# Performance work log

Hardware: AMD Instinct MI355X
Metric: run time of the kernel (lower is better)

## Reference

```python
import jax, jax.numpy as jnp
import numpy as np

D = 768           # PTM hidden size
BS = 64           # block size
HEADS = D // BS   # 12 = bilinear blocks = EGAT heads = PTM attention heads
R = 97            # relation_num
B = 4; L = 1024; M = 48; NE = 24
P = NE * (NE - 1)
NEG = 0.2         # DGL EGATConv leaky_relu slope


def _make_hts():
    hh, tt = np.meshgrid(np.arange(NE), np.arange(NE), indexing='ij')
    keep = hh.reshape(-1) != tt.reshape(-1)
    return jnp.asarray(np.stack([hh.reshape(-1)[keep], tt.reshape(-1)[keep]], 0), jnp.int32)


def setup_inputs():
    key = jax.random.key(0)
    ks = jax.random.split(key, 20)
    context = jax.random.normal(ks[0], (B, L, D), jnp.float32) * 0.5
    att = jax.random.uniform(ks[1], (B, HEADS, L, L), jnp.float32)
    attention = att / att.sum(-1, keepdims=True)  # softmax-like rows
    mention_map = jnp.sort(jax.random.randint(ks[2], (B, M), 0, L, jnp.int32), axis=-1)
    assign = jnp.arange(M) % NE  # every entity owns >= 1 mention (avoids log(0))
    entity_map = jnp.tile(jax.nn.one_hot(assign, NE, dtype=jnp.float32).T[None], (B, 1, 1))
    hts = _make_hts()
    def lin(k, fi, fo):
        return jax.random.normal(k, (fi, fo), jnp.float32) * 0.02
    return dict(
        context=context, attention=attention, mention_map=mention_map,
        entity_map=entity_map, hts=hts,
        Whb=lin(ks[3], 2 * D, D), bhb=jnp.zeros((D,), jnp.float32),
        Wtb=lin(ks[4], 2 * D, D), btb=jnp.zeros((D,), jnp.float32),
        Wbin=lin(ks[5], D * BS, 2), bbin=jnp.zeros((2,), jnp.float32),
        Wrel=lin(ks[6], D * BS, R), brel=jnp.zeros((R,), jnp.float32),
        Wh=lin(ks[7], 2 * D, D), bh=jnp.zeros((D,), jnp.float32),
        Wt=lin(ks[8], 2 * D, D), bt=jnp.zeros((D,), jnp.float32),
        Wnode=lin(ks[9], D, HEADS * BS), Wni=lin(ks[10], D, HEADS * BS),
        Wfij=lin(ks[11], D, HEADS * BS), Wnj=lin(ks[12], D, HEADS * BS),
        attn_p=jax.random.normal(ks[13], (HEADS, BS), jnp.float32) * 0.1,
        egat_b=jnp.zeros((HEADS * BS,), jnp.float32),
    )


def _gbl(x1, x2, W, b):
    # group_biLinear: blockwise outer product then linear
    n = x1.shape[0]
    a = x1.reshape(n, HEADS, BS)
    c = x2.reshape(n, HEADS, BS)
    return jnp.einsum('nhi,nhj->nhij', a, c).reshape(n, -1) @ W + b


def reference(context, attention, mention_map, entity_map, hts,
              Whb, bhb, Wtb, btb, Wbin, bbin, Wrel, brel,
              Wh, bh, Wt, bt, Wnode, Wni, Wfij, Wnj, attn_p, egat_b):
    Bn = context.shape[0]
    bidx = jnp.arange(Bn)[:, None]
    # ---- get_ht: logsumexp mention->entity pooling ----
    men = context[bidx, mention_map]                                        # [B,M,D]
    entity = jnp.log(jnp.einsum('bnm,bmd->bnd', entity_map, jnp.exp(men)))  # [B,NE,D]
    h = entity[:, hts[0]].reshape(Bn * P, D)
    t = entity[:, hts[1]].reshape(Bn * P, D)
    # ---- context_pooling ----
    att_m = jnp.take_along_axis(attention, mention_map[:, None, :, None], axis=2)  # [B,H,M,L]
    cur = jnp.einsum('bnm,bhml->bhnl', entity_map, att_m)                   # [B,H,NE,L]
    cur = cur / (entity_map.sum(-1)[:, None, :, None] + 1e-20)
    ca = (cur[:, :, hts[0]] * cur[:, :, hts[1]]).sum(1)                     # [B,P,L]
    ca = ca / (ca.sum(-1, keepdims=True) + 1e-20)
    ci = jnp.einsum('bpl,bld->bpd', ca, context)                            # [B,P,D]
    ci_f = ci.reshape(Bn * P, D)
    # ---- binary classifier ----
    bin_h = jnp.tanh(jnp.concatenate([h, ci_f], -1) @ Whb + bhb)
    bin_t = jnp.tanh(jnp.concatenate([t, ci_f], -1) @ Wtb + btb)
    bin_res = _gbl(bin_h, bin_t, Wbin, bbin)                                # [B*P,2]
    # ---- graph build (masked uniform graph instead of ragged dgl graphs) ----
    mask = (jnp.argmax(bin_res, -1) == 1).reshape(Bn, P)                    # detached in torch
    src = jnp.concatenate([hts[0], jnp.arange(NE, dtype=hts.dtype)])        # self loops appended
    dst = jnp.concatenate([hts[1], jnp.arange(NE, dtype=hts.dtype)])

    def egat(nodes, ef, m):
        ef_all = jnp.concatenate([ef, jnp.zeros((NE, D), ef.dtype)], 0)     # zero self-loop feats
        m_all = jnp.concatenate([m, jnp.ones((NE,), bool)], 0)
        f_out = (nodes @ Wni)[src] + (nodes @ Wnj)[dst] + ef_all @ Wfij + egat_b
        f_out = f_out.reshape(-1, HEADS, BS)                                # [E,H,bs]
        score = (jax.nn.leaky_relu(f_out, NEG) * attn_p).sum(-1)            # [E,H]
        score = jnp.where(m_all[:, None], score, -1e30)
        smax = jax.ops.segment_max(score, dst, num_segments=NE)
        ex = jnp.exp(score - smax[dst]) * m_all[:, None]
        den = jax.ops.segment_sum(ex, dst, num_segments=NE)
        a = ex / (den[dst] + 1e-20)                                         # edge softmax per dst
        hsrc = (nodes @ Wnode).reshape(NE, HEADS, BS)
        nout = jax.ops.segment_sum(hsrc[src] * a[:, :, None], dst, num_segments=NE)
        return nout.reshape(NE, HEADS * BS), f_out[:P].reshape(P, HEADS * BS)

    node_out, ef_new = jax.vmap(egat)(entity, ci, mask)
    # ---- get_res: real edges take EGAT edge feats, non-edges keep context_info ----
    new_ci = jnp.where(mask[..., None], ef_new, ci).reshape(Bn * P, D)
    nh = node_out[:, hts[0]].reshape(Bn * P, D)
    nt = node_out[:, hts[1]].reshape(Bn * P, D)
    nh = jnp.tanh(jnp.concatenate([nh, new_ci], -1) @ Wh + bh)
    nt = jnp.tanh(jnp.concatenate([nt, new_ci], -1) @ Wt + bt)
    relation_res = _gbl(nh, nt, Wrel, brel)                                 # [B*P,97]
    return (bin_res, relation_res)
```

## Files before the change

kernel.cpp:

```cpp
#include <hip/hip_runtime.h>
#include <hip/hip_bf16.h>

#define Bn   4
#define Lq   1024
#define Dm   768
#define Mm   48
#define NEe  24
#define Pp   552
#define Ee   576
#define Hh   12
#define BSz  64
#define Rr   97
#define Nn   2208
#define NPAD 112
#define NEG_SLOPE 0.2f

typedef short bf16x8 __attribute__((ext_vector_type(8)));
typedef float f32x4  __attribute__((ext_vector_type(4)));

static __device__ __forceinline__ ushort f2b(float x) {
    __hip_bfloat16 h = __float2bfloat16(x);
    return *reinterpret_cast<ushort*>(&h);
}
static __device__ __forceinline__ float b2f(ushort h) {
    uint u = ((uint)h) << 16;
    return __uint_as_float(u);
}
static __device__ __forceinline__ void split2(float x, ushort& h, ushort& l) {
    h = f2b(x);
    l = f2b(x - b2f(h));
}

__global__ void k_entity(const float* __restrict__ ctx, const int* __restrict__ mmap,
                         const float* __restrict__ emap, float* __restrict__ entity,
                         ushort* __restrict__ entH, ushort* __restrict__ entL)
{
    int x = blockIdx.x;
    int b = x / NEe;
    int rows[8]; float wts[8]; int nnz = 0;
    for (int m = 0; m < Mm; ++m) {
        float w = emap[(long)x * Mm + m];
        if (w != 0.f && nnz < 8) { rows[nnz] = mmap[b * Mm + m]; wts[nnz] = w; ++nnz; }
    }
    const float* cbase = ctx + (long)b * Lq * Dm;
    for (int d = threadIdx.x; d < Dm; d += 256) {
        float s = 0.f;
        for (int z = 0; z < nnz; ++z) s += wts[z] * expf(cbase[(long)rows[z] * Dm + d]);
        float v = logf(s);
        entity[(long)x * Dm + d] = v;
        ushort hh, ll; split2(v, hh, ll);
        entH[(long)x * Dm + d] = hh;
        entL[(long)x * Dm + d] = ll;
    }
}

__global__ void k_cur(const float* __restrict__ att, const int* __restrict__ mmap,
                      const float* __restrict__ emap, float* __restrict__ cur)
{
    int x = blockIdx.x;
    int b = x / (Hh * NEe); int rem = x % (Hh * NEe);
    int h = rem / NEe;      int n = rem % NEe;
    float cnt = 0.f;
    int rows[8]; float wts[8]; int nnz = 0;
    for (int m = 0; m < Mm; ++m) {
        float w = emap[((long)b * NEe + n) * Mm + m];
        cnt += w;
        if (w != 0.f && nnz < 8) { rows[nnz] = mmap[b * Mm + m]; wts[nnz] = w; ++nnz; }
    }
    float inv = 1.f / (cnt + 1e-20f);
    const float* abase = att + ((long)b * Hh + h) * (long)Lq * Lq;
    float* obase = cur + (long)x * Lq;
    for (int l = threadIdx.x; l < Lq; l += 256) {
        float s = 0.f;
        for (int z = 0; z < nnz; ++z) s += wts[z] * abase[(long)rows[z] * Lq + l];
        obase[l] = s * inv;
    }
}

__global__ void k_ca(const float* __restrict__ cur, const int* __restrict__ hts,
                     ushort* __restrict__ caH, ushort* __restrict__ caL)
{
    int bp = blockIdx.x; int b = bp / Pp, p = bp % Pp;
    int n0 = hts[p], n1 = hts[Pp + p];
    __shared__ float red[256];
    float vals[4]; float lsum = 0.f;
    for (int t = 0; t < 4; ++t) {
        int l = threadIdx.x + t * 256;
        float v = 0.f;
        #pragma unroll
        for (int h = 0; h < Hh; ++h) {
            v += cur[(((long)b * Hh + h) * NEe + n0) * Lq + l] *
                 cur[(((long)b * Hh + h) * NEe + n1) * Lq + l];
        }
        vals[t] = v; lsum += v;
    }
    red[threadIdx.x] = lsum; __syncthreads();
    for (int s = 128; s > 0; s >>= 1) {
        if (threadIdx.x < s) red[threadIdx.x] += red[threadIdx.x + s];
        __syncthreads();
    }
    float inv = 1.f / (red[0] + 1e-20f);
    for (int t = 0; t < 4; ++t) {
        int l = threadIdx.x + t * 256;
        float v = vals[t] * inv;
        long idx = (long)bp * Lq + l;
        ushort hh, ll; split2(v, hh, ll);
        caH[idx] = hh; caL[idx] = ll;
    }
}

__global__ __launch_bounds__(256)
void k_gemm_split(const float* __restrict__ A, const float* __restrict__ W,
                  const float* __restrict__ bias, float* __restrict__ C,
                  int M, int N, int K, int lda, int ldw, int ldc,
                  long sA, long sW, long sC, int act)
{
    A += (long)blockIdx.z * sA;
    W += (long)blockIdx.z * sW;
    C += (long)blockIdx.z * sC;
    __shared__ ushort Ah[64][40], Al[64][40], Bh[64][40], Bl[64][40];
    const int tid = threadIdx.x;
    const int r0 = blockIdx.y * 64, c0 = blockIdx.x * 64;
    const int w = tid >> 6, l = tid & 63, lr = l & 15, lk = l >> 4;
    const int wr = (w >> 1) * 32, wc = (w & 1) * 32;
    f32x4 acc[2][2];
    #pragma unroll
    for (int m = 0; m < 2; ++m)
        #pragma unroll
        for (int n = 0; n < 2; ++n) acc[m][n] = (f32x4){0.f, 0.f, 0.f, 0.f};

    const int ar  = tid >> 3;
    const int kq  = (tid & 7) * 4;
    const int bkk = tid >> 4;
    const int cc4 = (tid & 15) * 4;
    const float4 z4 = make_float4(0.f, 0.f, 0.f, 0.f);

    for (int k0 = 0; k0 < K; k0 += 32) {
        #pragma unroll
        for (int s = 0; s < 2; ++s) {
            int r = ar + s * 32;
            int gr = r0 + r;
            float4 v = (gr < M) ? *(const float4*)&A[(long)gr * lda + k0 + kq] : z4;
            ushort h0, l0, h1, l1;
            split2(v.x, h0, l0); split2(v.y, h1, l1);
            *(uint*)&Ah[r][kq]     = (uint)h0 | ((uint)h1 << 16);
            *(uint*)&Al[r][kq]     = (uint)l0 | ((uint)l1 << 16);
            split2(v.z, h0, l0); split2(v.w, h1, l1);
            *(uint*)&Ah[r][kq + 2] = (uint)h0 | ((uint)h1 << 16);
            *(uint*)&Al[r][kq + 2] = (uint)l0 | ((uint)l1 << 16);
        }
        #pragma unroll
        for (int s = 0; s < 2; ++s) {
            int kk = bkk + s * 16;
            float4 v = *(const float4*)&W[(long)(k0 + kk) * ldw + c0 + cc4];
            ushort hh, ll;
            split2(v.x, hh, ll); Bh[cc4 + 0][kk] = hh; Bl[cc4 + 0][kk] = ll;
            split2(v.y, hh, ll); Bh[cc4 + 1][kk] = hh; Bl[cc4 + 1][kk] = ll;
            split2(v.z, hh, ll); Bh[cc4 + 2][kk] = hh; Bl[cc4 + 2][kk] = ll;
            split2(v.w, hh, ll); Bh[cc4 + 3][kk] = hh; Bl[cc4 + 3][kk] = ll;
        }
        __syncthreads();
        bf16x8 fah[2], fal[2], fbh[2], fbl[2];
        #pragma unroll
        for (int m = 0; m < 2; ++m) {
            fah[m] = *(const bf16x8*)&Ah[wr + m * 16 + lr][lk * 8];
            fal[m] = *(const bf16x8*)&Al[wr + m * 16 + lr][lk * 8];
        }
        #pragma unroll
        for (int n = 0; n < 2; ++n) {
            fbh[n] = *(const bf16x8*)&Bh[wc + n * 16 + lr][lk * 8];
            fbl[n] = *(const bf16x8*)&Bl[wc + n * 16 + lr][lk * 8];
        }
        #pragma unroll
        for (int m = 0; m < 2; ++m)
            #pragma unroll
            for (int n = 0; n < 2; ++n) {
                acc[m][n] = __builtin_amdgcn_mfma_f32_16x16x32_bf16(fal[m], fbh[n], acc[m][n], 0, 0, 0);
                acc[m][n] = __builtin_amdgcn_mfma_f32_16x16x32_bf16(fah[m], fbl[n], acc[m][n], 0, 0, 0);
                acc[m][n] = __builtin_amdgcn_mfma_f32_16x16x32_bf16(fah[m], fbh[n], acc[m][n], 0, 0, 0);
            }
        __syncthreads();
    }
    #pragma unroll
    for (int m = 0; m < 2; ++m) {
        #pragma unroll
        for (int q = 0; q < 4; ++q) {
            int gr = r0 + wr + m * 16 + lk * 4 + q;
            if (gr >= M) continue;
            #pragma unroll
            for (int n = 0; n < 2; ++n) {
                int gc = c0 + wc + n * 16 + lr;
                float v = acc[m][n][q] + (bias ? bias[gc] : 0.f);
                if (act) v = tanhf(v);
                C[(long)gr * ldc + gc] = v;
            }
        }
    }
}

__global__ __launch_bounds__(256)
void k_gemm3_64(const ushort* __restrict__ AH, const ushort* __restrict__ AL,
                const ushort* __restrict__ BH, const ushort* __restrict__ BL,
                const float* __restrict__ bias, float* __restrict__ C,
                ushort* __restrict__ Ch, ushort* __restrict__ Cl,
                int M, int N, int K, int ldc, int act,
                long sA, long sB, long sC)
{
    AH += blockIdx.z * sA; AL += blockIdx.z * sA;
    BH += blockIdx.z * sB; BL += blockIdx.z * sB;
    C  += blockIdx.z * sC;
    ushort* ChB = Ch ? Ch + blockIdx.z * sC : (ushort*)nullptr;
    ushort* ClB = Cl ? Cl + blockIdx.z * sC : (ushort*)nullptr;
    __shared__ ushort AsH[64][40], AsL[64][40], BsH[64][40], BsL[64][40];
    const int tid = threadIdx.x;
    const int r0 = blockIdx.y * 64, c0 = blockIdx.x * 64;
    const int w = tid >> 6, l = tid & 63, lr = l & 15, lk = l >> 4;
    const int wr = (w >> 1) * 32, wc = (w & 1) * 32;
    f32x4 acc[2][2];
    #pragma unroll
    for (int m = 0; m < 2; ++m)
        #pragma unroll
        for (int n = 0; n < 2; ++n) acc[m][n] = (f32x4){0.f, 0.f, 0.f, 0.f};

    const int srow = tid >> 2, scb = (tid & 1) * 16;
    const bool doB = (tid >> 1) & 1;
    const bool ok = doB ? (c0 + srow < N) : (r0 + srow < M);
    const long g = doB ? (long)(c0 + srow) : (long)(r0 + srow);
    const ushort* pH = (doB ? BH : AH) + (ok ? g : 0) * (long)K;
    const ushort* pL = (doB ? BL : AL) + (ok ? g : 0) * (long)K;
    ushort (*dH)[40] = doB ? BsH : AsH;
    ushort (*dL)[40] = doB ? BsL : AsL;
    const uint4 z4 = make_uint4(0, 0, 0, 0);
    for (int k0 = 0; k0 < K; k0 += 32) {
        int kc = k0 + scb;
        *(uint4*)&dH[srow][scb]     = ok ? *(const uint4*)&pH[kc]     : z4;
        *(uint4*)&dH[srow][scb + 8] = ok ? *(const uint4*)&pH[kc + 8] : z4;
        *(uint4*)&dL[srow][scb]     = ok ? *(const uint4*)&pL[kc]     : z4;
        *(uint4*)&dL[srow][scb + 8] = ok ? *(const uint4*)&pL[kc + 8] : z4;
        __syncthreads();
        bf16x8 ah[2], al_[2], bh[2], bl_[2];
        #pragma unroll
        for (int m = 0; m < 2; ++m) {
            ah[m]  = *(const bf16x8*)&AsH[wr + m * 16 + lr][lk * 8];
            al_[m] = *(const bf16x8*)&AsL[wr + m * 16 + lr][lk * 8];
        }
        #pragma unroll
        for (int n = 0; n < 2; ++n) {
            bh[n]  = *(const bf16x8*)&BsH[wc + n * 16 + lr][lk * 8];
            bl_[n] = *(const bf16x8*)&BsL[wc + n * 16 + lr][lk * 8];
        }
        #pragma unroll
        for (int m = 0; m < 2; ++m)
            #pragma unroll
            for (int n = 0; n < 2; ++n) {
                acc[m][n] = __builtin_amdgcn_mfma_f32_16x16x32_bf16(al_[m], bh[n], acc[m][n], 0, 0, 0);
                acc[m][n] = __builtin_amdgcn_mfma_f32_16x16x32_bf16(ah[m], bl_[n], acc[m][n], 0, 0, 0);
                acc[m][n] = __builtin_amdgcn_mfma_f32_16x16x32_bf16(ah[m], bh[n], acc[m][n], 0, 0, 0);
            }
        __syncthreads();
    }
    #pragma unroll
    for (int m = 0; m < 2; ++m) {
        #pragma unroll
        for (int q = 0; q < 4; ++q) {
            int gr = r0 + wr + m * 16 + lk * 4 + q;
            if (gr >= M) continue;
            #pragma unroll
            for (int n = 0; n < 2; ++n) {
                int gc = c0 + wc + n * 16 + lr;
                float v = acc[m][n][q] + (bias ? bias[gc] : 0.f);
                if (act) v = tanhf(v);
                long oi = (long)gr * ldc + gc;
                C[oi] = v;
                if (ChB) { ushort hh, ll; split2(v, hh, ll); ChB[oi] = hh; ClB[oi] = ll; }
            }
        }
    }
}

__global__ __launch_bounds__(256)
void k_gemm3_cat64(const ushort* __restrict__ ndH, const ushort* __restrict__ ndL,
                   const ushort* __restrict__ ftH, const ushort* __restrict__ ftL,
                   const int* __restrict__ hts,
                   const ushort* __restrict__ BH0, const ushort* __restrict__ BL0,
                   const ushort* __restrict__ BH1, const ushort* __restrict__ BL1,
                   const float* __restrict__ bias0, const float* __restrict__ bias1,
                   float* __restrict__ C0, float* __restrict__ C1)
{
    const int zz = blockIdx.z;
    const int* sel = hts + (zz ? Pp : 0);
    const ushort* BH = zz ? BH1 : BH0;
    const ushort* BL = zz ? BL1 : BL0;
    const float* bias = zz ? bias1 : bias0;
    float* C = zz ? C1 : C0;
    __shared__ ushort AsH[64][40], AsL[64][40], BsH[64][40], BsL[64][40];
    const int tid = threadIdx.x;
    const int r0 = blockIdx.y * 64, c0 = blockIdx.x * 64;
    const int w = tid >> 6, l = tid & 63, lr = l & 15, lk = l >> 4;
    const int wr = (w >> 1) * 32, wc = (w & 1) * 32;
    f32x4 acc[2][2];
    #pragma unroll
    for (int m = 0; m < 2; ++m)
        #pragma unroll
        for (int n = 0; n < 2; ++n) acc[m][n] = (f32x4){0.f, 0.f, 0.f, 0.f};

    const int srow = tid >> 2, scb = (tid & 1) * 16;
    const bool doB = (tid >> 1) & 1;
    const ushort *pH0, *pL0, *pH1, *pL1;
    bool ok;
    if (doB) {
        long gc = c0 + srow;
        ok = true;
        pH0 = BH + gc * (long)(2 * Dm); pL0 = BL + gc * (long)(2 * Dm);
        pH1 = pH0; pL1 = pL0;
    } else {
        int gra = r0 + srow;
        ok = gra < Nn;
        int grc = ok ? gra : Nn - 1;
        int b = grc / Pp, p = grc % Pp;
        pH0 = ndH + ((long)b * NEe + sel[p]) * Dm;
        pL0 = ndL + ((long)b * NEe + sel[p]) * Dm;
        pH1 = ftH + (long)grc * Dm - Dm;
        pL1 = ftL + (long)grc * Dm - Dm;
    }
    ushort (*dH)[40] = doB ? BsH : AsH;
    ushort (*dL)[40] = doB ? BsL : AsL;
    const uint4 z4 = make_uint4(0, 0, 0, 0);
    for (int k0 = 0; k0 < 2 * Dm; k0 += 32) {
        const ushort* sH = ((k0 < Dm) ? pH0 : pH1) + k0 + scb;
        const ushort* sL = ((k0 < Dm) ? pL0 : pL1) + k0 + scb;
        *(uint4*)&dH[srow][scb]     = ok ? *(const uint4*)sH       : z4;
        *(uint4*)&dH[srow][scb + 8] = ok ? *(const uint4*)(sH + 8) : z4;
        *(uint4*)&dL[srow][scb]     = ok ? *(const uint4*)sL       : z4;
        *(uint4*)&dL[srow][scb + 8] = ok ? *(const uint4*)(sL + 8) : z4;
        __syncthreads();
        bf16x8 ah[2], al_[2], bh[2], bl_[2];
        #pragma unroll
        for (int m = 0; m < 2; ++m) {
            ah[m]  = *(const bf16x8*)&AsH[wr + m * 16 + lr][lk * 8];
            al_[m] = *(const bf16x8*)&AsL[wr + m * 16 + lr][lk * 8];
        }
        #pragma unroll
        for (int n = 0; n < 2; ++n) {
            bh[n]  = *(const bf16x8*)&BsH[wc + n * 16 + lr][lk * 8];
            bl_[n] = *(const bf16x8*)&BsL[wc + n * 16 + lr][lk * 8];
        }
        #pragma unroll
        for (int m = 0; m < 2; ++m)
            #pragma unroll
            for (int n = 0; n < 2; ++n) {
                acc[m][n] = __builtin_amdgcn_mfma_f32_16x16x32_bf16(al_[m], bh[n], acc[m][n], 0, 0, 0);
                acc[m][n] = __builtin_amdgcn_mfma_f32_16x16x32_bf16(ah[m], bl_[n], acc[m][n], 0, 0, 0);
                acc[m][n] = __builtin_amdgcn_mfma_f32_16x16x32_bf16(ah[m], bh[n], acc[m][n], 0, 0, 0);
            }
        __syncthreads();
    }
    #pragma unroll
    for (int m = 0; m < 2; ++m) {
        #pragma unroll
        for (int q = 0; q < 4; ++q) {
            int gr = r0 + wr + m * 16 + lk * 4 + q;
            if (gr >= Nn) continue;
            #pragma unroll
            for (int n = 0; n < 2; ++n) {
                int gc = c0 + wc + n * 16 + lr;
                C[(long)gr * Dm + gc] = tanhf(acc[m][n][q] + bias[gc]);
            }
        }
    }
}

__global__ __launch_bounds__(256)
void k_gemm_bf64(const ushort* __restrict__ A, const ushort* __restrict__ Bt,
                 float* __restrict__ C, int M, int N, int K, int ldc)
{
    __shared__ ushort As[64][40], Bs[64][40];
    const int tid = threadIdx.x;
    const int r0 = blockIdx.y * 64, c0 = blockIdx.x * 64;
    const int w = tid >> 6, l = tid & 63, lr = l & 15, lk = l >> 4;
    const int wr = (w >> 1) * 32, wc = (w & 1) * 32;
    f32x4 acc[2][2];
    #pragma unroll
    for (int m = 0; m < 2; ++m)
        #pragma unroll
        for (int n = 0; n < 2; ++n) acc[m][n] = (f32x4){0.f, 0.f, 0.f, 0.f};

    const int srow = tid >> 2, scb = (tid & 1) * 16;
    const bool doB = (tid >> 1) & 1;
    const bool ok = doB ? (c0 + srow < N) : (r0 + srow < M);
    const long g = doB ? (long)(c0 + srow) : (long)(r0 + srow);
    const ushort* p = (doB ? Bt : A) + (ok ? g : 0) * (long)K;
    ushort (*d)[40] = doB ? Bs : As;
    const uint4 z4 = make_uint4(0, 0, 0, 0);
    for (int k0 = 0; k0 < K; k0 += 32) {
        int kc = k0 + scb;
        *(uint4*)&d[srow][scb]     = ok ? *(const uint4*)&p[kc]     : z4;
        *(uint4*)&d[srow][scb + 8] = ok ? *(const uint4*)&p[kc + 8] : z4;
        __syncthreads();
        bf16x8 af[2], bf_[2];
        #pragma unroll
        for (int m = 0; m < 2; ++m) af[m]  = *(const bf16x8*)&As[wr + m * 16 + lr][lk * 8];
        #pragma unroll
        for (int n = 0; n < 2; ++n) bf_[n] = *(const bf16x8*)&Bs[wc + n * 16 + lr][lk * 8];
        #pragma unroll
        for (int m = 0; m < 2; ++m)
            #pragma unroll
            for (int n = 0; n < 2; ++n)
                acc[m][n] = __builtin_amdgcn_mfma_f32_16x16x32_bf16(af[m], bf_[n], acc[m][n], 0, 0, 0);
        __syncthreads();
    }
    #pragma unroll
    for (int m = 0; m < 2; ++m) {
        #pragma unroll
        for (int q = 0; q < 4; ++q) {
            int gr = r0 + wr + m * 16 + lk * 4 + q;
            if (gr >= M) continue;
            #pragma unroll
            for (int n = 0; n < 2; ++n) {
                int gc = c0 + wc + n * 16 + lr;
                C[(long)gr * ldc + gc] = acc[m][n][q];
            }
        }
    }
}

__global__ __launch_bounds__(256)
void k_gemm_bf_cat64(const ushort* __restrict__ nodes, const ushort* __restrict__ feat,
                     const int* __restrict__ hts,
                     const ushort* __restrict__ Bt0, const ushort* __restrict__ Bt1,
                     const float* __restrict__ bias0, const float* __restrict__ bias1,
                     float* __restrict__ C0, float* __restrict__ C1)
{
    const int zz = blockIdx.z;
    const int* sel = hts + (zz ? Pp : 0);
    const ushort* Bt = zz ? Bt1 : Bt0;
    const float* bias = zz ? bias1 : bias0;
    float* C = zz ? C1 : C0;
    __shared__ ushort As[64][40], Bs[64][40];
    const int tid = threadIdx.x;
    const int r0 = blockIdx.y * 64, c0 = blockIdx.x * 64;
    const int w = tid >> 6, l = tid & 63, lr = l & 15, lk = l >> 4;
    const int wr = (w >> 1) * 32, wc = (w & 1) * 32;
    f32x4 acc[2][2];
    #pragma unroll
    for (int m = 0; m < 2; ++m)
        #pragma unroll
        for (int n = 0; n < 2; ++n) acc[m][n] = (f32x4){0.f, 0.f, 0.f, 0.f};

    const int srow = tid >> 2, scb = (tid & 1) * 16;
    const bool doB = (tid >> 1) & 1;
    const ushort *p0, *p1;
    bool ok;
    if (doB) {
        long gc = c0 + srow;
        ok = true;
        p0 = Bt + gc * (long)(2 * Dm);
        p1 = p0;
    } else {
        int gra = r0 + srow;
        ok = gra < Nn;
        int grc = ok ? gra : Nn - 1;
        int b = grc / Pp, p = grc % Pp;
        p0 = nodes + ((long)b * NEe + sel[p]) * Dm;
        p1 = feat + (long)grc * Dm - Dm;
    }
    ushort (*d)[40] = doB ? Bs : As;
    const uint4 z4 = make_uint4(0, 0, 0, 0);
    for (int k0 = 0; k0 < 2 * Dm; k0 += 32) {
        const ushort* s = ((k0 < Dm) ? p0 : p1) + k0 + scb;
        *(uint4*)&d[srow][scb]     = ok ? *(const uint4*)s       : z4;
        *(uint4*)&d[srow][scb + 8] = ok ? *(const uint4*)(s + 8) : z4;
        __syncthreads();
        bf16x8 af[2], bf_[2];
        #pragma unroll
        for (int m = 0; m < 2; ++m) af[m]  = *(const bf16x8*)&As[wr + m * 16 + lr][lk * 8];
        #pragma unroll
        for (int n = 0; n < 2; ++n) bf_[n] = *(const bf16x8*)&Bs[wc + n * 16 + lr][lk * 8];
        #pragma unroll
        for (int m = 0; m < 2; ++m)
            #pragma unroll
            for (int n = 0; n < 2; ++n)
                acc[m][n] = __builtin_amdgcn_mfma_f32_16x16x32_bf16(af[m], bf_[n], acc[m][n], 0, 0, 0);
        __syncthreads();
    }
    #pragma unroll
    for (int m = 0; m < 2; ++m) {
        #pragma unroll
        for (int q = 0; q < 4; ++q) {
            int gr = r0 + wr + m * 16 + lk * 4 + q;
            if (gr >= Nn) continue;
            #pragma unroll
            for (int n = 0; n < 2; ++n) {
                int gc = c0 + wc + n * 16 + lr;
                C[(long)gr * Dm + gc] = tanhf(acc[m][n][q] + bias[gc]);
            }
        }
    }
}

__global__ void k_wbinT(const float* __restrict__ W, float* __restrict__ out)
{
    int h = blockIdx.x;
    for (int idx = threadIdx.x; idx < 64 * 128; idx += 256) {
        int j = idx >> 7, io = idx & 127;
        int i = io >> 1, o = io & 1;
        out[(long)h * 64 * 128 + idx] = W[(((long)h * 64 + i) * 64 + j) * 2 + o];
    }
}

__global__ void k_binred(const float* __restrict__ act1, const float* __restrict__ T,
                         const float* __restrict__ bias, float* __restrict__ out0,
                         int* __restrict__ maskb)
{
    int w = threadIdx.x >> 6, l = threadIdx.x & 63;
    int n = blockIdx.x * 4 + w;
    if (n >= Nn) return;
    float a0 = 0.f, a1 = 0.f;
    #pragma unroll
    for (int h = 0; h < Hh; ++h) {
        float a = act1[(long)n * Dm + h * 64 + l];
        const float* t = T + ((long)(h * Nn + n)) * 128 + l * 2;
        a0 += a * t[0];
        a1 += a * t[1];
    }
    #pragma unroll
    for (int off = 32; off > 0; off >>= 1) {
        a0 += __shfl_down(a0, off);
        a1 += __shfl_down(a1, off);
    }
    if (l == 0) {
        float v0 = a0 + bias[0], v1 = a1 + bias[1];
        out0[n * 2 + 0] = v0;
        out0[n * 2 + 1] = v1;
        maskb[n] = v1 > v0 ? 1 : 0;
    }
}

__global__ void k_wT4(const float* __restrict__ i0, const float* __restrict__ i1,
                      const float* __restrict__ i2, const float* __restrict__ i3,
                      ushort* __restrict__ o0, ushort* __restrict__ o1,
                      ushort* __restrict__ o2, ushort* __restrict__ o3)
{
    const float* in; ushort* out;
    switch (blockIdx.z) {
        case 0: in = i0; out = o0; break;
        case 1: in = i1; out = o1; break;
        case 2: in = i2; out = o2; break;
        default: in = i3; out = o3; break;
    }
    __shared__ float t[32][33];
    int k0 = blockIdx.y * 32, n0 = blockIdx.x * 32;
    int tx = threadIdx.x & 31, ty = threadIdx.x >> 5;
    #pragma unroll
    for (int s = 0; s < 4; ++s)
        t[ty + s * 8][tx] = in[(long)(k0 + ty + s * 8) * Dm + n0 + tx];
    __syncthreads();
    #pragma unroll
    for (int s = 0; s < 4; ++s)
        out[(long)(n0 + ty + s * 8) * Dm + k0 + tx] = f2b(t[tx][ty + s * 8]);
}

__global__ void k_wT2(const float* __restrict__ i0, const float* __restrict__ i1,
                      ushort* __restrict__ o0, ushort* __restrict__ o1, int K, int N)
{
    const float* in = blockIdx.z ? i1 : i0;
    ushort* out = blockIdx.z ? o1 : o0;
    __shared__ float t[32][33];
    int k0 = blockIdx.y * 32, n0 = blockIdx.x * 32;
    int tx = threadIdx.x & 31, ty = threadIdx.x >> 5;
    #pragma unroll
    for (int s = 0; s < 4; ++s)
        t[ty + s * 8][tx] = in[(long)(k0 + ty + s * 8) * N + n0 + tx];
    __syncthreads();
    #pragma unroll
    for (int s = 0; s < 4; ++s)
        out[(long)(n0 + ty + s * 8) * K + k0 + tx] = f2b(t[tx][ty + s * 8]);
}

__global__ void k_wT_split2(const float* __restrict__ i0, const float* __restrict__ i1,
                            ushort* __restrict__ oH0, ushort* __restrict__ oL0,
                            ushort* __restrict__ oH1, ushort* __restrict__ oL1,
                            int K, int N)
{
    const float* in = blockIdx.z ? i1 : i0;
    ushort* outH = blockIdx.z ? oH1 : oH0;
    ushort* outL = blockIdx.z ? oL1 : oL0;
    __shared__ float t[32][33];
    int k0 = blockIdx.y * 32, n0 = blockIdx.x * 32;
    int tx = threadIdx.x & 31, ty = threadIdx.x >> 5;
    #pragma unroll
    for (int s = 0; s < 4; ++s)
        t[ty + s * 8][tx] = in[(long)(k0 + ty + s * 8) * N + n0 + tx];
    __syncthreads();
    #pragma unroll
    for (int s = 0; s < 4; ++s) {
        float v = t[tx][ty + s * 8];
        ushort hh, ll; split2(v, hh, ll);
        long oi = (long)(n0 + ty + s * 8) * K + k0 + tx;
        outH[oi] = hh;
        outL[oi] = ll;
    }
}

__global__ void k_ctx_split(const float* __restrict__ ctx, ushort* __restrict__ outH,
                            ushort* __restrict__ outL)
{
    const float* in = ctx + (long)blockIdx.z * Lq * Dm;
    ushort* oH = outH + (long)blockIdx.z * Dm * Lq;
    ushort* oL = outL + (long)blockIdx.z * Dm * Lq;
    __shared__ float t[32][33];
    int k0 = blockIdx.y * 32, n0 = blockIdx.x * 32;
    int tx = threadIdx.x & 31, ty = threadIdx.x >> 5;
    #pragma unroll
    for (int s = 0; s < 4; ++s)
        t[ty + s * 8][tx] = in[(long)(k0 + ty + s * 8) * Dm + n0 + tx];
    __syncthreads();
    #pragma unroll
    for (int s = 0; s < 4; ++s) {
        float v = t[tx][ty + s * 8];
        ushort hh, ll; split2(v, hh, ll);
        long oi = (long)(n0 + ty + s * 8) * Lq + k0 + tx;
        oH[oi] = hh;
        oL[oi] = ll;
    }
}

__global__ void k_wrelT(const float* __restrict__ W, ushort* __restrict__ out)
{
    int hi = blockIdx.x;
    for (int idx = threadIdx.x; idx < NPAD * 64; idx += 256) {
        int o = idx >> 6, j = idx & 63;
        float v = (o < Rr) ? W[((long)hi * 64 + j) * Rr + o] : 0.f;
        out[(long)hi * NPAD * 64 + idx] = f2b(v);
    }
}

__global__ __launch_bounds__(256)
void k_gbl_mfma(const float* __restrict__ Aact, const float* __restrict__ Cact,
                const ushort* __restrict__ Wt, float* __restrict__ part)
{
    const int bid = blockIdx.x;
    const int xcd = bid & 7, sb = bid >> 3;
    int h, t;
    if (sb < 36) { h = xcd;             t = sb; }
    else         { h = 8 + (xcd >> 1);  t = (sb - 36) + 18 * (xcd & 1); }
    const int rb = t >> 1, jh = t & 1;
    const int r0 = rb * 128;
    const int j0 = jh * 32;
    __shared__ float a_s[128][68];
    const int tid = threadIdx.x;
    {
        int row = tid >> 1, cb = (tid & 1) * 32;
        long gr = r0 + row;
        if (gr < Nn) {
            const float* ap = Aact + gr * Dm + h * BSz + cb;
            #pragma unroll
            for (int q = 0; q < 32; q += 4)
                *(float4*)&a_s[row][cb + q] = *(const float4*)&ap[q];
        } else {
            #pragma unroll
            for (int q = 0; q < 32; ++q) a_s[row][cb + q] = 0.f;
        }
    }
    __syncthreads();
    const int w = tid >> 6, l = tid & 63, lr = l & 15, lk = l >> 4;
    const int wr = w * 32;
    f32x4 acc[2][7];
    #pragma unroll
    for (int m = 0; m < 2; ++m)
        #pragma unroll
        for (int n = 0; n < 7; ++n) acc[m][n] = (f32x4){0.f, 0.f, 0.f, 0.f};

    const ushort* wbase = Wt + (long)h * 64 * NPAD * 64;
    float cc[2][8];
    #pragma unroll
    for (int m = 0; m < 2; ++m) {
        int crow = r0 + wr + m * 16 + lr;
        if (crow >= Nn) crow = Nn - 1;
        const float* cp = Cact + (long)crow * Dm + h * BSz + j0 + lk * 8;
        float4 clo = *(const float4*)cp;
        float4 chi = *(const float4*)(cp + 4);
        cc[m][0] = clo.x; cc[m][1] = clo.y; cc[m][2] = clo.z; cc[m][3] = clo.w;
        cc[m][4] = chi.x; cc[m][5] = chi.y; cc[m][6] = chi.z; cc[m][7] = chi.w;
    }
    for (int i = 0; i < 64; ++i) {
        bf16x8 bfr[7];
        const ushort* wp = wbase + (long)i * NPAD * 64 + j0 + lk * 8;
        #pragma unroll
        for (int n = 0; n < 7; ++n)
            bfr[n] = *(const bf16x8*)(wp + (long)(n * 16 + lr) * 64);
        #pragma unroll
        for (int m = 0; m < 2; ++m) {
            float av = a_s[wr + m * 16 + lr][i];
            bf16x8 af;
            #pragma unroll
            for (int q = 0; q < 8; ++q)
                af[q] = (short)f2b(av * cc[m][q]);
            #pragma unroll
            for (int n = 0; n < 7; ++n)
                acc[m][n] = __builtin_amdgcn_mfma_f32_16x16x32_bf16(af, bfr[n], acc[m][n], 0, 0, 0);
        }
    }
    float* pdst = part + ((long)(h * 2 + jh) * Nn) * NPAD;
    #pragma unroll
    for (int m = 0; m < 2; ++m) {
        #pragma unroll
        for (int q = 0; q < 4; ++q) {
            int gr = r0 + wr + m * 16 + lk * 4 + q;
            if (gr >= Nn) continue;
            #pragma unroll
            for (int n = 0; n < 7; ++n) {
                int o = n * 16 + lr;
                pdst[(long)gr * NPAD + o] = acc[m][n][q];
            }
        }
    }
}

__global__ void k_rel_reduce(const float* __restrict__ part, const float* __restrict__ bias,
                             float* __restrict__ out)
{
    int idx = blockIdx.x * 256 + threadIdx.x;
    if (idx >= Nn * Rr) return;
    int n = idx / Rr, o = idx % Rr;
    float s = bias[o];
    #pragma unroll
    for (int h = 0; h < 2 * Hh; ++h) s += part[((long)h * Nn + n) * NPAD + o];
    out[idx] = s;
}

__global__ void k_fassemble_score(const float* __restrict__ fij, const float* __restrict__ ni,
                                  const float* __restrict__ nj, const float* __restrict__ eb,
                                  const int* __restrict__ hts, float* __restrict__ fout, int ldn,
                                  const float* __restrict__ attp, const int* __restrict__ mask,
                                  float* __restrict__ score)
{
    int be = blockIdx.x; int b = be / Ee, e = be % Ee;
    int sn, dn; const float* fe = nullptr;
    if (e < Pp) { sn = hts[e]; dn = hts[Pp + e]; fe = fij + ((long)b * Pp + e) * Dm; }
    else        { sn = dn = e - Pp; }
    const float* nib = ni + ((long)b * NEe + sn) * ldn;
    const float* njb = nj + ((long)b * NEe + dn) * ldn;
    float* ob = fout + (long)be * Dm;
    __shared__ float sd[Dm];
    for (int d = threadIdx.x; d < Dm; d += 256) {
        float v = (fe ? fe[d] : 0.f) + nib[d] + njb[d] + eb[d];
        ob[d] = v;
        float lr = v >= 0.f ? v : NEG_SLOPE * v;
        sd[d] = lr * attp[d];
    }
    __syncthreads();
    const int wv = threadIdx.x >> 6, ln = threadIdx.x & 63;
    const bool okm = (e >= Pp) || (mask[b * Pp + e] != 0);
    for (int h = wv; h < Hh; h += 4) {
        float s = sd[h * 64 + ln];
        #pragma unroll
        for (int off = 32; off > 0; off >>= 1) s += __shfl_down(s, off);
        if (ln == 0) score[(long)be * Hh + h] = okm ? s : -1e30f;
    }
}

__global__ void k_segsoft(const float* __restrict__ score, float* __restrict__ attw)
{
    int idx = blockIdx.x * 256 + threadIdx.x;
    if (idx >= Bn * NEe * Hh) return;
    int h = idx % Hh; int bnn = idx / Hh; int b = bnn / NEe, n = bnn % NEe;
    float sc[NEe]; int es[NEe];
    float smax = -3e38f;
    #pragma unroll
    for (int hh = 0; hh < NEe; ++hh) {
        int e;
        if (hh == n) e = Pp + n;
        else         e = hh * (NEe - 1) + (n - (n > hh ? 1 : 0));
        float v = score[((long)b * Ee + e) * Hh + h];
        es[hh] = e; sc[hh] = v;
        smax = fmaxf(smax, v);
    }
    float den = 0.f;
    #pragma unroll
    for (int z = 0; z < NEe; ++z) { sc[z] = expf(sc[z] - smax); den += sc[z]; }
    float inv = 1.f / (den + 1e-20f);
    #pragma unroll
    for (int z = 0; z < NEe; ++z)
        attw[((long)b * Ee + es[z]) * Hh + h] = sc[z] * inv;
}

__global__ void k_nodeout_bf(const float* __restrict__ hsrcB, const float* __restrict__ attw,
                             ushort* __restrict__ nout, int ldn)
{
    int bnn = blockIdx.x; int b = bnn / NEe, n = bnn % NEe;
    for (int d = threadIdx.x; d < Dm; d += 256) {
        int h = d >> 6;
        float s = 0.f;
        #pragma unroll
        for (int hh = 0; hh < NEe; ++hh) {
            int e, sn;
            if (hh == n) { e = Pp + n; sn = n; }
            else         { e = hh * (NEe - 1) + (n - (n > hh ? 1 : 0)); sn = hh; }
            s += hsrcB[((long)b * NEe + sn) * ldn + d] * attw[((long)b * Ee + e) * Hh + h];
        }
        nout[(long)bnn * Dm + d] = f2b(s);
    }
}

__global__ void k_newci_bf(const float* __restrict__ fout, const float* __restrict__ ci,
                           const int* __restrict__ mask, ushort* __restrict__ out)
{
    int idx = blockIdx.x * 256 + threadIdx.x;
    if (idx >= Nn * Dm) return;
    int n = idx / Dm, d = idx % Dm;
    int b = n / Pp, p = n % Pp;
    out[idx] = f2b(mask[n] ? fout[((long)b * Ee + p) * Dm + d] : ci[idx]);
}

extern "C" void kernel_launch(void* const* d_in, const int* in_sizes, int n_in,
                              void* d_out, int out_size, void* d_ws, size_t ws_size,
                              hipStream_t stream)
{
    const float* ctx   = (const float*)d_in[0];
    const float* att   = (const float*)d_in[1];
    const int*   mmap  = (const int*)d_in[2];
    const float* emap  = (const float*)d_in[3];
    const int*   hts   = (const int*)d_in[4];
    const float* Whb   = (const float*)d_in[5];
    const float* bhb   = (const float*)d_in[6];
    const float* Wtb   = (const float*)d_in[7];
    const float* btb   = (const float*)d_in[8];
    const float* Wbin  = (const float*)d_in[9];
    const float* bbin  = (const float*)d_in[10];
    const float* Wrel  = (const float*)d_in[11];
    const float* brel  = (const float*)d_in[12];
    const float* Wh    = (const float*)d_in[13];
    const float* bh    = (const float*)d_in[14];
    const float* Wt    = (const float*)d_in[15];
    const float* bt    = (const float*)d_in[16];
    const float* Wnode = (const float*)d_in[17];
    const float* Wni   = (const float*)d_in[18];
    const float* Wfij  = (const float*)d_in[19];
    const float* Wnj   = (const float*)d_in[20];
    const float* attp  = (const float*)d_in[21];
    const float* egatb = (const float*)d_in[22];

    float* out0 = (float*)d_out;
    float* out1 = out0 + (long)Nn * 2;

    float* w = (float*)d_ws;
    size_t off = 0;
    auto alloc = [&](size_t nf) { float* p = w + off; off += nf; return p; };
    float* entity = alloc((size_t)Bn * NEe * Dm);
    float* curb   = alloc((size_t)Bn * Hh * NEe * Lq);
    float* cab    = alloc((size_t)Bn * Pp * Lq);
    float* cib    = alloc((size_t)Nn * Dm);
    float* act1   = alloc((size_t)Nn * Dm);
    float* act2   = alloc((size_t)Nn * Dm);
    float* fijb   = alloc((size_t)Nn * Dm);
    float* foutb  = alloc((size_t)Bn * Ee * Dm);
    float* comb   = alloc((size_t)Bn * NEe * 3 * Dm);
    float* scoreb = alloc((size_t)Bn * Ee * Hh);
    float* attwb  = alloc((size_t)Bn * Ee * Hh);
    int*   maskb  = (int*)alloc(Nn);
    ushort* entbf = (ushort*)alloc((size_t)Bn * NEe * Dm / 2);
    ushort* cibbf = (ushort*)alloc((size_t)Nn * Dm / 2);
    ushort* WTe   = (ushort*)alloc((size_t)3 * Dm * Dm / 2);
    ushort* WfijT = (ushort*)alloc((size_t)Dm * Dm / 2);
    ushort* WhT   = (ushort*)alloc((size_t)Dm * 2 * Dm / 2);
    ushort* WtT   = (ushort*)alloc((size_t)Dm * 2 * Dm / 2);
    ushort* WrelB = (ushort*)alloc((size_t)Dm * NPAD * 64 / 2);
    float*  Wb2   = alloc((size_t)Hh * 64 * 128);
    ushort* entL  = (ushort*)alloc((size_t)Bn * NEe * Dm / 2);
    ushort* cibL  = (ushort*)alloc((size_t)Nn * Dm / 2);
    ushort* WhbTH = (ushort*)alloc((size_t)Dm * 2 * Dm / 2);
    ushort* WhbTL = (ushort*)alloc((size_t)Dm * 2 * Dm / 2);
    ushort* WtbTH = (ushort*)alloc((size_t)Dm * 2 * Dm / 2);
    ushort* WtbTL = (ushort*)alloc((size_t)Dm * 2 * Dm / 2);
    ushort* ctxTH = (ushort*)alloc((size_t)Bn * Dm * Lq / 2);
    ushort* ctxTL = (ushort*)alloc((size_t)Bn * Dm * Lq / 2);
    float*  part2 = alloc((size_t)2 * Hh * Nn * NPAD);
    float*  Tb      = curb;
    ushort* caH     = (ushort*)cab;
    ushort* caL     = caH + (size_t)Bn * Pp * Lq;
    ushort* noutbf  = entbf;
    ushort* newcibf = cibbf;

    k_wT4<<<dim3(24, 24, 4), 256, 0, stream>>>(Wni, Wnj, Wnode, Wfij,
        WTe, WTe + Dm * Dm, WTe + 2 * Dm * Dm, WfijT);
    k_wT2<<<dim3(24, 48, 2), 256, 0, stream>>>(Wh, Wt, WhT, WtT, 2 * Dm, Dm);
    k_wT_split2<<<dim3(24, 48, 2), 256, 0, stream>>>(Whb, Wtb, WhbTH, WhbTL,
                                                     WtbTH, WtbTL, 2 * Dm, Dm);
    k_ctx_split<<<dim3(24, 32, 4), 256, 0, stream>>>(ctx, ctxTH, ctxTL);
    k_wrelT<<<Dm, 256, 0, stream>>>(Wrel, WrelB);
    k_wbinT<<<Hh, 256, 0, stream>>>(Wbin, Wb2);

    k_entity<<<Bn * NEe, 256, 0, stream>>>(ctx, mmap, emap, entity, entbf, entL);
    k_cur<<<Bn * Hh * NEe, 256, 0, stream>>>(att, mmap, emap, curb);
    k_ca<<<Bn * Pp, 256, 0, stream>>>(curb, hts, caH, caL);
    k_gemm3_64<<<dim3(Dm / 64, (Pp + 63) / 64, Bn), 256, 0, stream>>>(
        caH, caL, ctxTH, ctxTL, nullptr, cib, cibbf, cibL,
        Pp, Dm, Lq, Dm, 0, (long)Pp * Lq, (long)Dm * Lq, (long)Pp * Dm);

    k_gemm3_cat64<<<dim3(Dm / 64, (Nn + 63) / 64, 2), 256, 0, stream>>>(
        entbf, entL, cibbf, cibL, hts,
        WhbTH, WhbTL, WtbTH, WtbTL, bhb, btb, act1, act2);
    k_gemm_split<<<dim3(2, (Nn + 63) / 64, Hh), 256, 0, stream>>>(
        act2, Wb2, nullptr, Tb, Nn, 128, 64, Dm, 128, 128,
        64L, 64L * 128, (long)Nn * 128, 0);
    k_binred<<<Nn / 4, 256, 0, stream>>>(act1, Tb, bbin, out0, maskb);

    k_gemm_bf64<<<dim3(3 * Dm / 64, 2), 256, 0, stream>>>(entbf, WTe, comb, Bn * NEe, 3 * Dm, Dm, 3 * Dm);
    k_gemm_bf64<<<dim3(Dm / 64, (Nn + 63) / 64), 256, 0, stream>>>(cibbf, WfijT, fijb, Nn, Dm, Dm, Dm);

    k_fassemble_score<<<Bn * Ee, 256, 0, stream>>>(fijb, comb, comb + Dm, egatb, hts,
                                                   foutb, 3 * Dm, attp, maskb, scoreb);
    k_segsoft<<<(Bn * NEe * Hh + 255) / 256, 256, 0, stream>>>(scoreb, attwb);
    k_nodeout_bf<<<Bn * NEe, 256, 0, stream>>>(comb + 2 * Dm, attwb, noutbf, 3 * Dm);
    k_newci_bf<<<(Nn * Dm + 255) / 256, 256, 0, stream>>>(foutb, cib, maskb, newcibf);

    k_gemm_bf_cat64<<<dim3(Dm / 64, (Nn + 63) / 64, 2), 256, 0, stream>>>(
        noutbf, newcibf, hts, WhT, WtT, bh, bt, act1, act2);

    k_gbl_mfma<<<432, 256, 0, stream>>>(act1, act2, WrelB, part2);
    k_rel_reduce<<<(Nn * Rr + 255) / 256, 256, 0, stream>>>(part2, brel, out1);

    (void)in_sizes; (void)n_in; (void)out_size; (void)ws_size;
}
```

Before: 426.3 us.

## Fuse EGAT softmax/nodeout and new-ci build; double-buffer weight loads in gbl MFMA

Merges the edge segment-softmax and node aggregation into a single kernel that keeps attention weights in shared memory, and folds the masked new-context-info bf16 conversion into the edge-feature assembly kernel. This removes two launches and the global round trip for the attention weights and edge features. It also software-pipelines the weight fragment loads in the group-bilinear MFMA kernel with a two-stage register buffer to hide load latency, which raises register pressure.

```diff
diff --git a/kernel.cpp b/kernel.cpp
--- a/kernel.cpp
+++ b/kernel.cpp
@@ -671,7 +671,7 @@
         #pragma unroll
         for (int n = 0; n < 7; ++n) acc[m][n] = (f32x4){0.f, 0.f, 0.f, 0.f};
 
-    const ushort* wbase = Wt + (long)h * 64 * NPAD * 64;
+    const ushort* wbase = Wt + (long)h * 64 * NPAD * 64 + j0 + lk * 8;
     float cc[2][8];
     #pragma unroll
     for (int m = 0; m < 2; ++m) {
@@ -683,12 +683,18 @@
         cc[m][0] = clo.x; cc[m][1] = clo.y; cc[m][2] = clo.z; cc[m][3] = clo.w;
         cc[m][4] = chi.x; cc[m][5] = chi.y; cc[m][6] = chi.z; cc[m][7] = chi.w;
     }
+    bf16x8 bfr[2][7];
+    #pragma unroll
+    for (int n = 0; n < 7; ++n)
+        bfr[0][n] = *(const bf16x8*)(wbase + (long)(n * 16 + lr) * 64);
     for (int i = 0; i < 64; ++i) {
-        bf16x8 bfr[7];
-        const ushort* wp = wbase + (long)i * NPAD * 64 + j0 + lk * 8;
-        #pragma unroll
-        for (int n = 0; n < 7; ++n)
-            bfr[n] = *(const bf16x8*)(wp + (long)(n * 16 + lr) * 64);
+        const int cur = i & 1;
+        if (i < 63) {
+            const ushort* wp = wbase + (long)(i + 1) * NPAD * 64;
+            #pragma unroll
+            for (int n = 0; n < 7; ++n)
+                bfr[cur ^ 1][n] = *(const bf16x8*)(wp + (long)(n * 16 + lr) * 64);
+        }
         #pragma unroll
         for (int m = 0; m < 2; ++m) {
             float av = a_s[wr + m * 16 + lr][i];
@@ -698,7 +704,7 @@
                 af[q] = (short)f2b(av * cc[m][q]);
             #pragma unroll
             for (int n = 0; n < 7; ++n)
-                acc[m][n] = __builtin_amdgcn_mfma_f32_16x16x32_bf16(af, bfr[n], acc[m][n], 0, 0, 0);
+                acc[m][n] = __builtin_amdgcn_mfma_f32_16x16x32_bf16(af, bfr[cur][n], acc[m][n], 0, 0, 0);
         }
     }
     float* pdst = part + ((long)(h * 2 + jh) * Nn) * NPAD;
@@ -733,7 +739,8 @@
                                   const float* __restrict__ nj, const float* __restrict__ eb,
                                   const int* __restrict__ hts, float* __restrict__ fout, int ldn,
                                   const float* __restrict__ attp, const int* __restrict__ mask,
-                                  float* __restrict__ score)
+                                  float* __restrict__ score,
+                                  const float* __restrict__ ci, ushort* __restrict__ newci)
 {
     int be = blockIdx.x; int b = be / Ee, e = be % Ee;
     int sn, dn; const float* fe = nullptr;
@@ -742,16 +749,19 @@
     const float* nib = ni + ((long)b * NEe + sn) * ldn;
     const float* njb = nj + ((long)b * NEe + dn) * ldn;
     float* ob = fout + (long)be * Dm;
+    const bool okm = (e >= Pp) || (mask[b * Pp + e] != 0);
+    const long nrow = (long)b * Pp + e;
     __shared__ float sd[Dm];
     for (int d = threadIdx.x; d < Dm; d += 256) {
         float v = (fe ? fe[d] : 0.f) + nib[d] + njb[d] + eb[d];
         ob[d] = v;
         float lr = v >= 0.f ? v : NEG_SLOPE * v;
         sd[d] = lr * attp[d];
+        if (e < Pp)
+            newci[nrow * Dm + d] = f2b(okm ? v : ci[nrow * Dm + d]);
     }
     __syncthreads();
     const int wv = threadIdx.x >> 6, ln = threadIdx.x & 63;
-    const bool okm = (e >= Pp) || (mask[b * Pp + e] != 0);
     for (int h = wv; h < Hh; h += 4) {
         float s = sd[h * 64 + ln];
         #pragma unroll
@@ -760,57 +770,41 @@
     }
 }
 
-__global__ void k_segsoft(const float* __restrict__ score, float* __restrict__ attw)
-{
-    int idx = blockIdx.x * 256 + threadIdx.x;
-    if (idx >= Bn * NEe * Hh) return;
-    int h = idx % Hh; int bnn = idx / Hh; int b = bnn / NEe, n = bnn % NEe;
-    float sc[NEe]; int es[NEe];
-    float smax = -3e38f;
-    #pragma unroll
-    for (int hh = 0; hh < NEe; ++hh) {
-        int e;
-        if (hh == n) e = Pp + n;
-        else         e = hh * (NEe - 1) + (n - (n > hh ? 1 : 0));
-        float v = score[((long)b * Ee + e) * Hh + h];
-        es[hh] = e; sc[hh] = v;
-        smax = fmaxf(smax, v);
-    }
-    float den = 0.f;
-    #pragma unroll
-    for (int z = 0; z < NEe; ++z) { sc[z] = expf(sc[z] - smax); den += sc[z]; }
-    float inv = 1.f / (den + 1e-20f);
-    #pragma unroll
-    for (int z = 0; z < NEe; ++z)
-        attw[((long)b * Ee + es[z]) * Hh + h] = sc[z] * inv;
-}
-
-__global__ void k_nodeout_bf(const float* __restrict__ hsrcB, const float* __restrict__ attw,
-                             ushort* __restrict__ nout, int ldn)
+__global__ void k_egat_att(const float* __restrict__ score, const float* __restrict__ hsrcB,
+                           ushort* __restrict__ nout, int ldn)
 {
     int bnn = blockIdx.x; int b = bnn / NEe, n = bnn % NEe;
-    for (int d = threadIdx.x; d < Dm; d += 256) {
+    __shared__ float aw[NEe][Hh + 1];
+    int tid = threadIdx.x;
+    if (tid < Hh) {
+        int h = tid;
+        float sc[NEe];
+        float smax = -3e38f;
+        #pragma unroll
+        for (int hh = 0; hh < NEe; ++hh) {
+            int e;
+            if (hh == n) e = Pp + n;
+            else         e = hh * (NEe - 1) + (n - (n > hh ? 1 : 0));
+            float v = score[((long)b * Ee + e) * Hh + h];
+            sc[hh] = v;
+            smax = fmaxf(smax, v);
+        }
+        float den = 0.f;
+        #pragma unroll
+        for (int z = 0; z < NEe; ++z) { sc[z] = expf(sc[z] - smax); den += sc[z]; }
+        float inv = 1.f / (den + 1e-20f);
+        #pragma unroll
+        for (int z = 0; z < NEe; ++z) aw[z][h] = sc[z] * inv;
+    }
+    __syncthreads();
+    for (int d = tid; d < Dm; d += 256) {
         int h = d >> 6;
         float s = 0.f;
         #pragma unroll
-        for (int hh = 0; hh < NEe; ++hh) {
-            int e, sn;
-            if (hh == n) { e = Pp + n; sn = n; }
-            else         { e = hh * (NEe - 1) + (n - (n > hh ? 1 : 0)); sn = hh; }
-            s += hsrcB[((long)b * NEe + sn) * ldn + d] * attw[((long)b * Ee + e) * Hh + h];
-        }
+        for (int hh = 0; hh < NEe; ++hh)
+            s += hsrcB[((long)b * NEe + hh) * ldn + d] * aw[hh][h];
         nout[(long)bnn * Dm + d] = f2b(s);
     }
-}
-
-__global__ void k_newci_bf(const float* __restrict__ fout, const float* __restrict__ ci,
-                           const int* __restrict__ mask, ushort* __restrict__ out)
-{
-    int idx = blockIdx.x * 256 + threadIdx.x;
-    if (idx >= Nn * Dm) return;
-    int n = idx / Dm, d = idx % Dm;
-    int b = n / Pp, p = n % Pp;
-    out[idx] = f2b(mask[n] ? fout[((long)b * Ee + p) * Dm + d] : ci[idx]);
 }
 
 extern "C" void kernel_launch(void* const* d_in, const int* in_sizes, int n_in,
@@ -881,6 +875,7 @@
     ushort* caL     = caH + (size_t)Bn * Pp * Lq;
     ushort* noutbf  = entbf;
     ushort* newcibf = cibbf;
+    (void)attwb;
 
     k_wT4<<<dim3(24, 24, 4), 256, 0, stream>>>(Wni, Wnj, Wnode, Wfij,
         WTe, WTe + Dm * Dm, WTe + 2 * Dm * Dm, WfijT);
@@ -910,10 +905,9 @@
     k_gemm_bf64<<<dim3(Dm / 64, (Nn + 63) / 64), 256, 0, stream>>>(cibbf, WfijT, fijb, Nn, Dm, Dm, Dm);
 
     k_fassemble_score<<<Bn * Ee, 256, 0, stream>>>(fijb, comb, comb + Dm, egatb, hts,
-                                                   foutb, 3 * Dm, attp, maskb, scoreb);
-    k_segsoft<<<(Bn * NEe * Hh + 255) / 256, 256, 0, stream>>>(scoreb, attwb);
-    k_nodeout_bf<<<Bn * NEe, 256, 0, stream>>>(comb + 2 * Dm, attwb, noutbf, 3 * Dm);
-    k_newci_bf<<<(Nn * Dm + 255) / 256, 256, 0, stream>>>(foutb, cib, maskb, newcibf);
+                                                   foutb, 3 * Dm, attp, maskb, scoreb,
+                                                   cib, newcibf);
+    k_egat_att<<<Bn * NEe, 256, 0, stream>>>(scoreb, comb + 2 * Dm, noutbf, 3 * Dm);
 
     k_gemm_bf_cat64<<<dim3(Dm / 64, (Nn + 63) / 64, 2), 256, 0, stream>>>(
         noutbf, newcibf, hts, WhT, WtT, bh, bt, act1, act2);
```

Result: slower. 570.3 us (+33.8%).
